# Kernel optimization log

Hardware: AMD Instinct MI355X
Metric: run time of the kernel (lower is better)

The kernel has to match this reference:

```python
import jax, jax.numpy as jnp
import numpy as np

N_GAUSS = 2048
FEAT_DIM = 3
IMG_H, IMG_W = 256, 256
EPS = 1e-4  # args.eps with tiled rasterizer path


def setup_inputs() -> dict:
    key = jax.random.key(0)
    k_xy, k_sc, k_rot, k_feat = jax.random.split(key, 4)
    xy = jax.random.uniform(k_xy, (N_GAUSS, 2), dtype=jnp.float32)  # normalized [0,1) coords
    # scale holds INVERSE std-devs (disable_inverse_scale=False path: scale = 1/init_scale);
    # values 10..50 give Gaussians spanning a few pixels at 256x256.
    scale = jax.random.uniform(k_sc, (N_GAUSS, 2), minval=10.0, maxval=50.0, dtype=jnp.float32)
    rot = jax.random.normal(k_rot, (N_GAUSS, 1), dtype=jnp.float32)
    feat = jax.random.uniform(k_feat, (N_GAUSS, FEAT_DIM), dtype=jnp.float32)
    return {"xy": xy, "scale": scale, "rot": rot, "feat": feat, "topk": 8}


def reference(xy, scale, rot, feat, topk):
    # Pixel centers in normalized coordinates, matching get_grid(h, w) -> (x, y)
    xs = (jnp.arange(IMG_W, dtype=jnp.float32) + 0.5) / IMG_W
    ys = (jnp.arange(IMG_H, dtype=jnp.float32) + 0.5) / IMG_H
    px, py = jnp.meshgrid(xs, ys, indexing="xy")  # each [H, W]
    px = px.reshape(-1)  # [P]
    py = py.reshape(-1)

    dx = px[:, None] - xy[None, :, 0]  # [P, N]
    dy = py[:, None] - xy[None, :, 1]  # [P, N]

    c = jnp.cos(rot[:, 0])  # [N]
    s = jnp.sin(rot[:, 0])
    # Rotate offset into the Gaussian's local frame
    lx = dx * c + dy * s   # [P, N]
    ly = -dx * s + dy * c  # [P, N]

    # Anisotropic Gaussian weight; scale is the inverse std-dev per axis
    w = jnp.exp(-0.5 * ((lx * scale[:, 0]) ** 2 + (ly * scale[:, 1]) ** 2))  # [P, N]

    # Keep top-k Gaussians per pixel, normalize their weights, accumulate features
    tw, ti = jax.lax.top_k(w, topk)        # [P, K]
    tf = feat[ti]                          # [P, K, C]
    alpha = tw / (jnp.sum(tw, axis=-1, keepdims=True) + EPS)  # [P, K]
    img = jnp.einsum("pk,pkc->pc", alpha, tf)                 # [P, C]
    return img.reshape(IMG_H, IMG_W, FEAT_DIM).transpose(2, 0, 1)  # [C, H, W]
```

## Files before the change

kernel.cpp:

```cpp
#include <hip/hip_runtime.h>
#include <math.h>

#define N_GAUSS 2048
#define IMG_H 256
#define IMG_W 256
#define NPIX (IMG_H * IMG_W)
#define EPS 1e-4f

#define TILE 8
#define TILES_X (IMG_W / TILE)
#define NTILES (TILES_X * (IMG_H / TILE))
#define SEG 512
#define D_HALF 0.019336f

#define LADDER(T, G)                                                     \
    if ((T) < v7) {                                                      \
        const bool c0 = (T) < v0, c1 = (T) < v1, c2 = (T) < v2;          \
        const bool c3 = (T) < v3, c4 = (T) < v4, c5 = (T) < v5;          \
        const bool c6 = (T) < v6;                                        \
        v7 = c6 ? v6 : (T);            i7 = c6 ? i6 : (G);               \
        v6 = c6 ? (c5 ? v5 : (T)) : v6; i6 = c6 ? (c5 ? i5 : (G)) : i6;  \
        v5 = c5 ? (c4 ? v4 : (T)) : v5; i5 = c5 ? (c4 ? i4 : (G)) : i5;  \
        v4 = c4 ? (c3 ? v3 : (T)) : v4; i4 = c4 ? (c3 ? i3 : (G)) : i4;  \
        v3 = c3 ? (c2 ? v2 : (T)) : v3; i3 = c3 ? (c2 ? i2 : (G)) : i3;  \
        v2 = c2 ? (c1 ? v1 : (T)) : v2; i2 = c2 ? (c1 ? i1 : (G)) : i2;  \
        v1 = c1 ? (c0 ? v0 : (T)) : v1; i1 = c1 ? (c0 ? i0 : (G)) : i1;  \
        v0 = c0 ? (T) : v0;            i0 = c0 ? (G) : i0;               \
    }

#define VLADDER(T)                                                       \
    if ((T) < v7) {                                                      \
        const bool c0 = (T) < v0, c1 = (T) < v1, c2 = (T) < v2;          \
        const bool c3 = (T) < v3, c4 = (T) < v4, c5 = (T) < v5;          \
        const bool c6 = (T) < v6;                                        \
        v7 = c6 ? v6 : (T);                                              \
        v6 = c6 ? (c5 ? v5 : (T)) : v6;                                  \
        v5 = c5 ? (c4 ? v4 : (T)) : v5;                                  \
        v4 = c4 ? (c3 ? v3 : (T)) : v4;                                  \
        v3 = c3 ? (c2 ? v2 : (T)) : v3;                                  \
        v2 = c2 ? (c1 ? v1 : (T)) : v2;                                  \
        v1 = c1 ? (c0 ? v0 : (T)) : v1;                                  \
        v0 = c0 ? (T) : v0;                                              \
    }

#define CE(a, i, j)                                   \
    { float lo_ = fminf(a[i], a[j]);                  \
      float hi_ = fmaxf(a[i], a[j]);                  \
      a[i] = lo_; a[j] = hi_; }

#define MERGE8(A, B)                                  \
    { float t_[8];                                    \
      t_[0] = fminf(A[0], B[7]); t_[1] = fminf(A[1], B[6]); \
      t_[2] = fminf(A[2], B[5]); t_[3] = fminf(A[3], B[4]); \
      t_[4] = fminf(A[4], B[3]); t_[5] = fminf(A[5], B[2]); \
      t_[6] = fminf(A[6], B[1]); t_[7] = fminf(A[7], B[0]); \
      CE(t_,0,4) CE(t_,1,5) CE(t_,2,6) CE(t_,3,7)     \
      CE(t_,0,2) CE(t_,1,3) CE(t_,4,6) CE(t_,5,7)     \
      CE(t_,0,1) CE(t_,2,3) CE(t_,4,5) CE(t_,6,7)     \
      A[0]=t_[0]; A[1]=t_[1]; A[2]=t_[2]; A[3]=t_[3]; \
      A[4]=t_[4]; A[5]=t_[5]; A[6]=t_[6]; A[7]=t_[7]; }

__launch_bounds__(256)
__global__ void fused_kernel(const float* __restrict__ xy,
                             const float* __restrict__ scale,
                             const float* __restrict__ rot,
                             const float* __restrict__ feat,
                             float* __restrict__ out) {
    __shared__ float rlo[N_GAUSS];
    __shared__ float wlist[4][8];
    __shared__ float s_cut;
    __shared__ unsigned short qidx[N_GAUSS];
    __shared__ int qcnt[4];
    __shared__ float          lt[4][8][64];
    __shared__ unsigned short li[4][8][64];

    const int tid  = threadIdx.x;
    const int lane = tid & 63;
    const int w    = tid >> 6;
    const int tile = blockIdx.x;

    const float cx = (float)((tile & (TILES_X - 1)) * TILE + 4) * (1.0f / IMG_W);
    const float cy = (float)((tile / TILES_X) * TILE + 4) * (1.0f / IMG_H);
    float cur[8];
    {
        float v0 = INFINITY, v1 = INFINITY, v2 = INFINITY, v3 = INFINITY;
        float v4 = INFINITY, v5 = INFINITY, v6 = INFINITY, v7 = INFINITY;
#pragma unroll
        for (int r = 0; r < N_GAUSS / 256; ++r) {
            int g = r * 256 + tid;
            float2 xyg = ((const float2*)xy)[g];
            float2 scg = ((const float2*)scale)[g];
            float  rg  = rot[g];
            float s, c;
            __sincosf(rg, &s, &c);
            float dx = cx - xyg.x;
            float dy = cy - xyg.y;
            float lx = dx * c + dy * s;
            float ly = dy * c - dx * s;
            float a  = lx * scg.x;
            float b  = ly * scg.y;
            float rr = sqrtf(a * a + b * b);
            float m  = fmaxf(scg.x, scg.y) * D_HALF;
            rlo[g]   = rr - m;
            float rp = rr + m;
            VLADDER(rp)
        }
        cur[0] = v0; cur[1] = v1; cur[2] = v2; cur[3] = v3;
        cur[4] = v4; cur[5] = v5; cur[6] = v6; cur[7] = v7;
    }

#pragma unroll
    for (int m = 1; m < 64; m <<= 1) {
        float oth[8];
#pragma unroll
        for (int k = 0; k < 8; ++k) oth[k] = __shfl_xor(cur[k], m, 64);
        float t_[8];
#pragma unroll
        for (int k = 0; k < 8; ++k) t_[k] = fminf(cur[k], oth[7 - k]);
        CE(t_,0,4) CE(t_,1,5) CE(t_,2,6) CE(t_,3,7)
        CE(t_,0,2) CE(t_,1,3) CE(t_,4,6) CE(t_,5,7)
        CE(t_,0,1) CE(t_,2,3) CE(t_,4,5) CE(t_,6,7)
#pragma unroll
        for (int k = 0; k < 8; ++k) cur[k] = t_[k];
    }
    if (lane == 0) {
#pragma unroll
        for (int k = 0; k < 8; ++k) wlist[w][k] = cur[k];
    }
    __syncthreads();

    if (tid == 0) {
        float A[8], B[8], C2[8], D2[8];
#pragma unroll
        for (int k = 0; k < 8; ++k) {
            A[k]  = wlist[0][k];
            B[k]  = wlist[1][k];
            C2[k] = wlist[2][k];
            D2[k] = wlist[3][k];
        }
        MERGE8(A, B)
        MERGE8(C2, D2)
        MERGE8(A, C2)
        float cut = A[7];
        s_cut = cut + 0.01f + 1e-4f * cut;
    }
    __syncthreads();
    const float cut = s_cut;

    {
        const int segbase = w * SEG;
        unsigned base = 0;
        for (int s2 = 0; s2 < SEG / 64; ++s2) {
            int g = segbase + s2 * 64 + lane;
            bool keep = rlo[g] <= cut;
            unsigned long long mask = __ballot(keep);
            unsigned pos = (unsigned)__popcll(mask & ((1ull << lane) - 1ull));
            if (keep) qidx[segbase + base + pos] = (unsigned short)g;
            base += (unsigned)__popcll(mask);
        }
        if (lane == 0) qcnt[w] = (int)base;
    }
    __syncthreads();

    const int pxi = (tile & (TILES_X - 1)) * TILE + (lane & 7);
    const int pyi = (tile / TILES_X) * TILE + (lane >> 3);
    const int p   = pyi * IMG_W + pxi;
    const float px = (pxi + 0.5f) * (1.0f / IMG_W);
    const float py = (pyi + 0.5f) * (1.0f / IMG_H);

    float v0 = INFINITY, v1 = INFINITY, v2 = INFINITY, v3 = INFINITY;
    float v4 = INFINITY, v5 = INFINITY, v6 = INFINITY, v7 = INFINITY;
    int   i0 = 0, i1 = 0, i2 = 0, i3 = 0, i4 = 0, i5 = 0, i6 = 0, i7 = 0;

    {
        const int segbase = w * SEG;
        const int cnt = qcnt[w];
        for (int b = 0; b < cnt; b += 64) {
            int t = b + lane;
            int gg = (t < cnt) ? (int)qidx[segbase + t] : 0;
            float2 xyg = ((const float2*)xy)[gg];
            float2 scg = ((const float2*)scale)[gg];
            double rg  = (double)rot[gg];
            float cc = (float)cos(rg);
            float ss = (float)sin(rg);
            int lim = cnt - b; if (lim > 64) lim = 64;
            for (int j = 0; j < lim; ++j) {
                float ax = __shfl(xyg.x, j, 64);
                float ay = __shfl(xyg.y, j, 64);
                float ac = __shfl(cc,    j, 64);
                float sn = __shfl(ss,    j, 64);
                float bx = __shfl(scg.x, j, 64);
                float by = __shfl(scg.y, j, 64);
                int   g  = __shfl(gg,    j, 64);
                float dx = __fsub_rn(px, ax);
                float dy = __fsub_rn(py, ay);
                float lx = __fadd_rn(__fmul_rn(dx, ac), __fmul_rn(dy, sn));
                float ly = __fadd_rn(__fmul_rn(-dx, sn), __fmul_rn(dy, ac));
                float aa = __fmul_rn(lx, bx);
                float bb = __fmul_rn(ly, by);
                float t2 = __fadd_rn(__fmul_rn(aa, aa), __fmul_rn(bb, bb));
                LADDER(t2, g)
            }
        }
    }

    lt[w][0][lane] = v0; li[w][0][lane] = (unsigned short)i0;
    lt[w][1][lane] = v1; li[w][1][lane] = (unsigned short)i1;
    lt[w][2][lane] = v2; li[w][2][lane] = (unsigned short)i2;
    lt[w][3][lane] = v3; li[w][3][lane] = (unsigned short)i3;
    lt[w][4][lane] = v4; li[w][4][lane] = (unsigned short)i4;
    lt[w][5][lane] = v5; li[w][5][lane] = (unsigned short)i5;
    lt[w][6][lane] = v6; li[w][6][lane] = (unsigned short)i6;
    lt[w][7][lane] = v7; li[w][7][lane] = (unsigned short)i7;
    __syncthreads();

    if (w == 0) {
        v0 = INFINITY; v1 = INFINITY; v2 = INFINITY; v3 = INFINITY;
        v4 = INFINITY; v5 = INFINITY; v6 = INFINITY; v7 = INFINITY;
        i0 = 0; i1 = 0; i2 = 0; i3 = 0; i4 = 0; i5 = 0; i6 = 0; i7 = 0;
        for (int c = 0; c < 4; ++c) {
#pragma unroll
            for (int k = 0; k < 8; ++k) {
                float t2 = lt[c][k][lane];
                int   g  = (int)li[c][k][lane];
                LADDER(t2, g)
            }
        }
        float w0 = expf(-0.5f * v0), w1 = expf(-0.5f * v1);
        float w2 = expf(-0.5f * v2), w3 = expf(-0.5f * v3);
        float w4 = expf(-0.5f * v4), w5 = expf(-0.5f * v5);
        float w6 = expf(-0.5f * v6), w7 = expf(-0.5f * v7);
        float sum = w0 + w1 + w2 + w3 + w4 + w5 + w6 + w7;
        float inv = 1.0f / (sum + EPS);

        float oc0 = 0.f, oc1 = 0.f, oc2 = 0.f;
#define ACC(K)                                                  \
        {                                                       \
            float al = w##K * inv;                              \
            const float* f = feat + 3 * i##K;                   \
            oc0 = fmaf(al, f[0], oc0);                          \
            oc1 = fmaf(al, f[1], oc1);                          \
            oc2 = fmaf(al, f[2], oc2);                          \
        }
        ACC(0) ACC(1) ACC(2) ACC(3) ACC(4) ACC(5) ACC(6) ACC(7)
#undef ACC

        out[p]            = oc0;
        out[p + NPIX]     = oc1;
        out[p + 2 * NPIX] = oc2;
    }
}

extern "C" void kernel_launch(void* const* d_in, const int* in_sizes, int n_in,
                              void* d_out, int out_size, void* d_ws, size_t ws_size,
                              hipStream_t stream) {
    const float* xy    = (const float*)d_in[0];
    const float* scale = (const float*)d_in[1];
    const float* rot   = (const float*)d_in[2];
    const float* feat  = (const float*)d_in[3];
    float* out = (float*)d_out;

    fused_kernel<<<NTILES, 256, 0, stream>>>(xy, scale, rot, feat, out);
}
```

Before: 24.74 us.

## Use 16x16 tiles with 1024-thread blocks and stage culled Gaussian params in LDS

```diff
diff --git a/kernel.cpp b/kernel.cpp
--- a/kernel.cpp
+++ b/kernel.cpp
@@ -7,11 +7,13 @@
 #define NPIX (IMG_H * IMG_W)
 #define EPS 1e-4f
 
-#define TILE 8
+#define TILE 16
 #define TILES_X (IMG_W / TILE)
 #define NTILES (TILES_X * (IMG_H / TILE))
-#define SEG 512
-#define D_HALF 0.019336f
+#define NTHREADS 1024
+#define NWAVES 16
+#define SEG (N_GAUSS / NWAVES)
+#define D_HALF 0.041436f
 
 #define LADDER(T, G)                                                     \
     if ((T) < v7) {                                                      \
@@ -48,46 +50,55 @@
       float hi_ = fmaxf(a[i], a[j]);                  \
       a[i] = lo_; a[j] = hi_; }
 
-#define MERGE8(A, B)                                  \
-    { float t_[8];                                    \
-      t_[0] = fminf(A[0], B[7]); t_[1] = fminf(A[1], B[6]); \
-      t_[2] = fminf(A[2], B[5]); t_[3] = fminf(A[3], B[4]); \
-      t_[4] = fminf(A[4], B[3]); t_[5] = fminf(A[5], B[2]); \
-      t_[6] = fminf(A[6], B[1]); t_[7] = fminf(A[7], B[0]); \
-      CE(t_,0,4) CE(t_,1,5) CE(t_,2,6) CE(t_,3,7)     \
-      CE(t_,0,2) CE(t_,1,3) CE(t_,4,6) CE(t_,5,7)     \
-      CE(t_,0,1) CE(t_,2,3) CE(t_,4,5) CE(t_,6,7)     \
-      A[0]=t_[0]; A[1]=t_[1]; A[2]=t_[2]; A[3]=t_[3]; \
-      A[4]=t_[4]; A[5]=t_[5]; A[6]=t_[6]; A[7]=t_[7]; }
-
-__launch_bounds__(256)
+__device__ __forceinline__ void top8_butterfly(float (&cur)[8]) {
+#pragma unroll
+    for (int m = 1; m < 64; m <<= 1) {
+        float oth[8];
+#pragma unroll
+        for (int k = 0; k < 8; ++k) oth[k] = __shfl_xor(cur[k], m, 64);
+        float t_[8];
+#pragma unroll
+        for (int k = 0; k < 8; ++k) t_[k] = fminf(cur[k], oth[7 - k]);
+        CE(t_,0,4) CE(t_,1,5) CE(t_,2,6) CE(t_,3,7)
+        CE(t_,0,2) CE(t_,1,3) CE(t_,4,6) CE(t_,5,7)
+        CE(t_,0,1) CE(t_,2,3) CE(t_,4,5) CE(t_,6,7)
+#pragma unroll
+        for (int k = 0; k < 8; ++k) cur[k] = t_[k];
+    }
+}
+
+__launch_bounds__(NTHREADS)
 __global__ void fused_kernel(const float* __restrict__ xy,
                              const float* __restrict__ scale,
                              const float* __restrict__ rot,
                              const float* __restrict__ feat,
                              float* __restrict__ out) {
     __shared__ float rlo[N_GAUSS];
-    __shared__ float wlist[4][8];
+    __shared__ float wlist[NWAVES][8];
     __shared__ float s_cut;
     __shared__ unsigned short qidx[N_GAUSS];
-    __shared__ int qcnt[4];
-    __shared__ float          lt[4][8][64];
-    __shared__ unsigned short li[4][8][64];
+    __shared__ int qcnt[NWAVES];
+    __shared__ float4 cps[N_GAUSS];
+    __shared__ float2 csc[N_GAUSS];
+    __shared__ float          lt[4][8][256];
+    __shared__ unsigned short li[4][8][256];
 
     const int tid  = threadIdx.x;
     const int lane = tid & 63;
     const int w    = tid >> 6;
     const int tile = blockIdx.x;
-
-    const float cx = (float)((tile & (TILES_X - 1)) * TILE + 4) * (1.0f / IMG_W);
-    const float cy = (float)((tile / TILES_X) * TILE + 4) * (1.0f / IMG_H);
+    const int tx   = tile & (TILES_X - 1);
+    const int ty   = tile >> 4;
+
+    const float cx = (float)(tx * TILE + 8) * (1.0f / IMG_W);
+    const float cy = (float)(ty * TILE + 8) * (1.0f / IMG_H);
     float cur[8];
     {
         float v0 = INFINITY, v1 = INFINITY, v2 = INFINITY, v3 = INFINITY;
         float v4 = INFINITY, v5 = INFINITY, v6 = INFINITY, v7 = INFINITY;
 #pragma unroll
-        for (int r = 0; r < N_GAUSS / 256; ++r) {
-            int g = r * 256 + tid;
+        for (int r = 0; r < N_GAUSS / NTHREADS; ++r) {
+            int g = r * NTHREADS + tid;
             float2 xyg = ((const float2*)xy)[g];
             float2 scg = ((const float2*)scale)[g];
             float  rg  = rot[g];
@@ -109,40 +120,23 @@
         cur[4] = v4; cur[5] = v5; cur[6] = v6; cur[7] = v7;
     }
 
-#pragma unroll
-    for (int m = 1; m < 64; m <<= 1) {
-        float oth[8];
-#pragma unroll
-        for (int k = 0; k < 8; ++k) oth[k] = __shfl_xor(cur[k], m, 64);
-        float t_[8];
-#pragma unroll
-        for (int k = 0; k < 8; ++k) t_[k] = fminf(cur[k], oth[7 - k]);
-        CE(t_,0,4) CE(t_,1,5) CE(t_,2,6) CE(t_,3,7)
-        CE(t_,0,2) CE(t_,1,3) CE(t_,4,6) CE(t_,5,7)
-        CE(t_,0,1) CE(t_,2,3) CE(t_,4,5) CE(t_,6,7)
-#pragma unroll
-        for (int k = 0; k < 8; ++k) cur[k] = t_[k];
-    }
+    top8_butterfly(cur);
     if (lane == 0) {
 #pragma unroll
         for (int k = 0; k < 8; ++k) wlist[w][k] = cur[k];
     }
     __syncthreads();
 
-    if (tid == 0) {
-        float A[8], B[8], C2[8], D2[8];
-#pragma unroll
-        for (int k = 0; k < 8; ++k) {
-            A[k]  = wlist[0][k];
-            B[k]  = wlist[1][k];
-            C2[k] = wlist[2][k];
-            D2[k] = wlist[3][k];
-        }
-        MERGE8(A, B)
-        MERGE8(C2, D2)
-        MERGE8(A, C2)
-        float cut = A[7];
-        s_cut = cut + 0.01f + 1e-4f * cut;
+    if (w == 0) {
+        float cur2[8];
+#pragma unroll
+        for (int k = 0; k < 8; ++k)
+            cur2[k] = (lane < NWAVES) ? wlist[lane][k] : INFINITY;
+        top8_butterfly(cur2);
+        if (lane == 0) {
+            float cut = cur2[7];
+            s_cut = cut + 0.01f + 1e-4f * cut;
+        }
     }
     __syncthreads();
     const float cut = s_cut;
@@ -154,16 +148,27 @@
             int g = segbase + s2 * 64 + lane;
             bool keep = rlo[g] <= cut;
             unsigned long long mask = __ballot(keep);
-            unsigned pos = (unsigned)__popcll(mask & ((1ull << lane) - 1ull));
-            if (keep) qidx[segbase + base + pos] = (unsigned short)g;
+            if (keep) {
+                unsigned pos = base + (unsigned)__popcll(mask & ((1ull << lane) - 1ull));
+                float2 xyg = ((const float2*)xy)[g];
+                float2 scg = ((const float2*)scale)[g];
+                double rg  = (double)rot[g];
+                float cc = (float)cos(rg);
+                float ss = (float)sin(rg);
+                qidx[segbase + pos] = (unsigned short)g;
+                cps[segbase + pos]  = make_float4(xyg.x, xyg.y, cc, ss);
+                csc[segbase + pos]  = make_float2(scg.x, scg.y);
+            }
             base += (unsigned)__popcll(mask);
         }
         if (lane == 0) qcnt[w] = (int)base;
     }
     __syncthreads();
 
-    const int pxi = (tile & (TILES_X - 1)) * TILE + (lane & 7);
-    const int pyi = (tile / TILES_X) * TILE + (lane >> 3);
+    const int st = w & 3;
+    const int q  = w >> 2;
+    const int pxi = tx * TILE + (st & 1) * 8 + (lane & 7);
+    const int pyi = ty * TILE + (st >> 1) * 8 + (lane >> 3);
     const int p   = pyi * IMG_W + pxi;
     const float px = (pxi + 0.5f) * (1.0f / IMG_W);
     const float py = (pyi + 0.5f) * (1.0f / IMG_H);
@@ -172,57 +177,47 @@
     float v4 = INFINITY, v5 = INFINITY, v6 = INFINITY, v7 = INFINITY;
     int   i0 = 0, i1 = 0, i2 = 0, i3 = 0, i4 = 0, i5 = 0, i6 = 0, i7 = 0;
 
+    for (int s = q * 4; s < q * 4 + 4; ++s) {
+        const int sb  = s * SEG;
+        const int cnt = qcnt[s];
+        for (int j = 0; j < cnt; ++j) {
+            float4 a4 = cps[sb + j];
+            float2 b2 = csc[sb + j];
+            int    g  = (int)qidx[sb + j];
+            float dx = __fsub_rn(px, a4.x);
+            float dy = __fsub_rn(py, a4.y);
+            float lx = __fadd_rn(__fmul_rn(dx, a4.z), __fmul_rn(dy, a4.w));
+            float ly = __fadd_rn(__fmul_rn(-dx, a4.w), __fmul_rn(dy, a4.z));
+            float aa = __fmul_rn(lx, b2.x);
+            float bb = __fmul_rn(ly, b2.y);
+            float t2 = __fadd_rn(__fmul_rn(aa, aa), __fmul_rn(bb, bb));
+            LADDER(t2, g)
+        }
+    }
+
     {
-        const int segbase = w * SEG;
-        const int cnt = qcnt[w];
-        for (int b = 0; b < cnt; b += 64) {
-            int t = b + lane;
-            int gg = (t < cnt) ? (int)qidx[segbase + t] : 0;
-            float2 xyg = ((const float2*)xy)[gg];
-            float2 scg = ((const float2*)scale)[gg];
-            double rg  = (double)rot[gg];
-            float cc = (float)cos(rg);
-            float ss = (float)sin(rg);
-            int lim = cnt - b; if (lim > 64) lim = 64;
-            for (int j = 0; j < lim; ++j) {
-                float ax = __shfl(xyg.x, j, 64);
-                float ay = __shfl(xyg.y, j, 64);
-                float ac = __shfl(cc,    j, 64);
-                float sn = __shfl(ss,    j, 64);
-                float bx = __shfl(scg.x, j, 64);
-                float by = __shfl(scg.y, j, 64);
-                int   g  = __shfl(gg,    j, 64);
-                float dx = __fsub_rn(px, ax);
-                float dy = __fsub_rn(py, ay);
-                float lx = __fadd_rn(__fmul_rn(dx, ac), __fmul_rn(dy, sn));
-                float ly = __fadd_rn(__fmul_rn(-dx, sn), __fmul_rn(dy, ac));
-                float aa = __fmul_rn(lx, bx);
-                float bb = __fmul_rn(ly, by);
-                float t2 = __fadd_rn(__fmul_rn(aa, aa), __fmul_rn(bb, bb));
-                LADDER(t2, g)
-            }
-        }
-    }
-
-    lt[w][0][lane] = v0; li[w][0][lane] = (unsigned short)i0;
-    lt[w][1][lane] = v1; li[w][1][lane] = (unsigned short)i1;
-    lt[w][2][lane] = v2; li[w][2][lane] = (unsigned short)i2;
-    lt[w][3][lane] = v3; li[w][3][lane] = (unsigned short)i3;
-    lt[w][4][lane] = v4; li[w][4][lane] = (unsigned short)i4;
-    lt[w][5][lane] = v5; li[w][5][lane] = (unsigned short)i5;
-    lt[w][6][lane] = v6; li[w][6][lane] = (unsigned short)i6;
-    lt[w][7][lane] = v7; li[w][7][lane] = (unsigned short)i7;
-    __syncthreads();
-
-    if (w == 0) {
+        const int pix = st * 64 + lane;
+        lt[q][0][pix] = v0; li[q][0][pix] = (unsigned short)i0;
+        lt[q][1][pix] = v1; li[q][1][pix] = (unsigned short)i1;
+        lt[q][2][pix] = v2; li[q][2][pix] = (unsigned short)i2;
+        lt[q][3][pix] = v3; li[q][3][pix] = (unsigned short)i3;
+        lt[q][4][pix] = v4; li[q][4][pix] = (unsigned short)i4;
+        lt[q][5][pix] = v5; li[q][5][pix] = (unsigned short)i5;
+        lt[q][6][pix] = v6; li[q][6][pix] = (unsigned short)i6;
+        lt[q][7][pix] = v7; li[q][7][pix] = (unsigned short)i7;
+    }
+    __syncthreads();
+
+    if (w < 4) {
         v0 = INFINITY; v1 = INFINITY; v2 = INFINITY; v3 = INFINITY;
         v4 = INFINITY; v5 = INFINITY; v6 = INFINITY; v7 = INFINITY;
         i0 = 0; i1 = 0; i2 = 0; i3 = 0; i4 = 0; i5 = 0; i6 = 0; i7 = 0;
+        const int pix = w * 64 + lane;
         for (int c = 0; c < 4; ++c) {
 #pragma unroll
             for (int k = 0; k < 8; ++k) {
-                float t2 = lt[c][k][lane];
-                int   g  = (int)li[c][k][lane];
+                float t2 = lt[c][k][pix];
+                int   g  = (int)li[c][k][pix];
                 LADDER(t2, g)
             }
         }
@@ -260,5 +255,5 @@
     const float* feat  = (const float*)d_in[3];
     float* out = (float*)d_out;
 
-    fused_kernel<<<NTILES, 256, 0, stream>>>(xy, scale, rot, feat, out);
+    fused_kernel<<<NTILES, NTHREADS, 0, stream>>>(xy, scale, rot, feat, out);
 }
```

Result: slower. 26.80 us (+8.3%).

## Precompute per-Gaussian params in prep kernel and stage candidates in LDS

Applied to the files above, without the earlier changes.

```diff
diff --git a/kernel.cpp b/kernel.cpp
--- a/kernel.cpp
+++ b/kernel.cpp
@@ -11,6 +11,7 @@
 #define TILES_X (IMG_W / TILE)
 #define NTILES (TILES_X * (IMG_H / TILE))
 #define SEG 512
+#define SEGCAP 128
 #define D_HALF 0.019336f
 
 #define LADDER(T, G)                                                     \
@@ -28,25 +29,18 @@
         v0 = c0 ? (T) : v0;            i0 = c0 ? (G) : i0;               \
     }
 
-#define VLADDER(T)                                                       \
-    if ((T) < v7) {                                                      \
-        const bool c0 = (T) < v0, c1 = (T) < v1, c2 = (T) < v2;          \
-        const bool c3 = (T) < v3, c4 = (T) < v4, c5 = (T) < v5;          \
-        const bool c6 = (T) < v6;                                        \
-        v7 = c6 ? v6 : (T);                                              \
-        v6 = c6 ? (c5 ? v5 : (T)) : v6;                                  \
-        v5 = c5 ? (c4 ? v4 : (T)) : v5;                                  \
-        v4 = c4 ? (c3 ? v3 : (T)) : v4;                                  \
-        v3 = c3 ? (c2 ? v2 : (T)) : v3;                                  \
-        v2 = c2 ? (c1 ? v1 : (T)) : v2;                                  \
-        v1 = c1 ? (c0 ? v0 : (T)) : v1;                                  \
-        v0 = c0 ? (T) : v0;                                              \
-    }
-
 #define CE(a, i, j)                                   \
     { float lo_ = fminf(a[i], a[j]);                  \
       float hi_ = fmaxf(a[i], a[j]);                  \
       a[i] = lo_; a[j] = hi_; }
+
+#define SORT8(a)                                      \
+    CE(a,0,1) CE(a,2,3) CE(a,4,5) CE(a,6,7)           \
+    CE(a,0,2) CE(a,1,3) CE(a,4,6) CE(a,5,7)           \
+    CE(a,1,2) CE(a,5,6)                               \
+    CE(a,0,4) CE(a,1,5) CE(a,2,6) CE(a,3,7)           \
+    CE(a,2,4) CE(a,3,5)                               \
+    CE(a,1,2) CE(a,3,4) CE(a,5,6)
 
 #define MERGE8(A, B)                                  \
     { float t_[8];                                    \
@@ -60,10 +54,48 @@
       A[0]=t_[0]; A[1]=t_[1]; A[2]=t_[2]; A[3]=t_[3]; \
       A[4]=t_[4]; A[5]=t_[5]; A[6]=t_[6]; A[7]=t_[7]; }
 
+__device__ __forceinline__ void top8_butterfly(float (&cur)[8]) {
+#pragma unroll
+    for (int m = 1; m < 64; m <<= 1) {
+        float oth[8];
+#pragma unroll
+        for (int k = 0; k < 8; ++k) oth[k] = __shfl_xor(cur[k], m, 64);
+        float t_[8];
+#pragma unroll
+        for (int k = 0; k < 8; ++k) t_[k] = fminf(cur[k], oth[7 - k]);
+        CE(t_,0,4) CE(t_,1,5) CE(t_,2,6) CE(t_,3,7)
+        CE(t_,0,2) CE(t_,1,3) CE(t_,4,6) CE(t_,5,7)
+        CE(t_,0,1) CE(t_,2,3) CE(t_,4,5) CE(t_,6,7)
+#pragma unroll
+        for (int k = 0; k < 8; ++k) cur[k] = t_[k];
+    }
+}
+
+__global__ void prep_kernel(const float* __restrict__ xy,
+                            const float* __restrict__ scale,
+                            const float* __restrict__ rot,
+                            float4* __restrict__ gA,
+                            float4* __restrict__ gB,
+                            float4* __restrict__ gC) {
+    int g = blockIdx.x * blockDim.x + threadIdx.x;
+    if (g >= N_GAUSS) return;
+    float x  = xy[2 * g + 0];
+    float y  = xy[2 * g + 1];
+    float sx = scale[2 * g + 0];
+    float sy = scale[2 * g + 1];
+    double r = (double)rot[g];
+    float c = (float)cos(r);
+    float s = (float)sin(r);
+    gA[g] = make_float4(x, y, c * sx, s * sx);
+    gB[g] = make_float4(-s * sy, c * sy, fmaxf(sx, sy) * D_HALF, 0.f);
+    gC[g] = make_float4(c, s, sx, sy);
+}
+
 __launch_bounds__(256)
 __global__ void fused_kernel(const float* __restrict__ xy,
-                             const float* __restrict__ scale,
-                             const float* __restrict__ rot,
+                             const float4* __restrict__ gA,
+                             const float4* __restrict__ gB,
+                             const float4* __restrict__ gC,
                              const float* __restrict__ feat,
                              float* __restrict__ out) {
     __shared__ float rlo[N_GAUSS];
@@ -71,6 +103,8 @@
     __shared__ float s_cut;
     __shared__ unsigned short qidx[N_GAUSS];
     __shared__ int qcnt[4];
+    __shared__ float4 cps[4 * SEGCAP];
+    __shared__ float2 csc[4 * SEGCAP];
     __shared__ float          lt[4][8][64];
     __shared__ unsigned short li[4][8][64];
 
@@ -82,47 +116,22 @@
     const float cx = (float)((tile & (TILES_X - 1)) * TILE + 4) * (1.0f / IMG_W);
     const float cy = (float)((tile / TILES_X) * TILE + 4) * (1.0f / IMG_H);
     float cur[8];
-    {
-        float v0 = INFINITY, v1 = INFINITY, v2 = INFINITY, v3 = INFINITY;
-        float v4 = INFINITY, v5 = INFINITY, v6 = INFINITY, v7 = INFINITY;
-#pragma unroll
-        for (int r = 0; r < N_GAUSS / 256; ++r) {
-            int g = r * 256 + tid;
-            float2 xyg = ((const float2*)xy)[g];
-            float2 scg = ((const float2*)scale)[g];
-            float  rg  = rot[g];
-            float s, c;
-            __sincosf(rg, &s, &c);
-            float dx = cx - xyg.x;
-            float dy = cy - xyg.y;
-            float lx = dx * c + dy * s;
-            float ly = dy * c - dx * s;
-            float a  = lx * scg.x;
-            float b  = ly * scg.y;
-            float rr = sqrtf(a * a + b * b);
-            float m  = fmaxf(scg.x, scg.y) * D_HALF;
-            rlo[g]   = rr - m;
-            float rp = rr + m;
-            VLADDER(rp)
-        }
-        cur[0] = v0; cur[1] = v1; cur[2] = v2; cur[3] = v3;
-        cur[4] = v4; cur[5] = v5; cur[6] = v6; cur[7] = v7;
-    }
-
-#pragma unroll
-    for (int m = 1; m < 64; m <<= 1) {
-        float oth[8];
-#pragma unroll
-        for (int k = 0; k < 8; ++k) oth[k] = __shfl_xor(cur[k], m, 64);
-        float t_[8];
-#pragma unroll
-        for (int k = 0; k < 8; ++k) t_[k] = fminf(cur[k], oth[7 - k]);
-        CE(t_,0,4) CE(t_,1,5) CE(t_,2,6) CE(t_,3,7)
-        CE(t_,0,2) CE(t_,1,3) CE(t_,4,6) CE(t_,5,7)
-        CE(t_,0,1) CE(t_,2,3) CE(t_,4,5) CE(t_,6,7)
-#pragma unroll
-        for (int k = 0; k < 8; ++k) cur[k] = t_[k];
-    }
+#pragma unroll
+    for (int r = 0; r < N_GAUSS / 256; ++r) {
+        int g = r * 256 + tid;
+        float4 a = gA[g];
+        float4 b = gB[g];
+        float dx = cx - a.x;
+        float dy = cy - a.y;
+        float lx = dx * a.z + dy * a.w;
+        float ly = dx * b.x + dy * b.y;
+        float rr = sqrtf(lx * lx + ly * ly);
+        rlo[g]  = rr - b.z;
+        cur[r]  = rr + b.z;
+    }
+    SORT8(cur)
+
+    top8_butterfly(cur);
     if (lane == 0) {
 #pragma unroll
         for (int k = 0; k < 8; ++k) wlist[w][k] = cur[k];
@@ -154,8 +163,16 @@
             int g = segbase + s2 * 64 + lane;
             bool keep = rlo[g] <= cut;
             unsigned long long mask = __ballot(keep);
-            unsigned pos = (unsigned)__popcll(mask & ((1ull << lane) - 1ull));
-            if (keep) qidx[segbase + base + pos] = (unsigned short)g;
+            if (keep) {
+                unsigned pos = base + (unsigned)__popcll(mask & ((1ull << lane) - 1ull));
+                qidx[segbase + pos] = (unsigned short)g;
+                if (pos < SEGCAP) {
+                    float4 a = gA[g];
+                    float4 e = gC[g];
+                    cps[w * SEGCAP + pos] = make_float4(a.x, a.y, e.x, e.y);
+                    csc[w * SEGCAP + pos] = make_float2(e.z, e.w);
+                }
+            }
             base += (unsigned)__popcll(mask);
         }
         if (lane == 0) qcnt[w] = (int)base;
@@ -172,37 +189,36 @@
     float v4 = INFINITY, v5 = INFINITY, v6 = INFINITY, v7 = INFINITY;
     int   i0 = 0, i1 = 0, i2 = 0, i3 = 0, i4 = 0, i5 = 0, i6 = 0, i7 = 0;
 
+#define PROC_EXACT(AX, AY, AC, AS, BX, BY, G)                            \
+    {                                                                    \
+        float dx = __fsub_rn(px, (AX));                                  \
+        float dy = __fsub_rn(py, (AY));                                  \
+        float lx = __fadd_rn(__fmul_rn(dx, (AC)), __fmul_rn(dy, (AS)));  \
+        float ly = __fadd_rn(__fmul_rn(-dx, (AS)), __fmul_rn(dy, (AC))); \
+        float aa = __fmul_rn(lx, (BX));                                  \
+        float bb = __fmul_rn(ly, (BY));                                  \
+        float t2 = __fadd_rn(__fmul_rn(aa, aa), __fmul_rn(bb, bb));      \
+        LADDER(t2, (G))                                                  \
+    }
+
     {
         const int segbase = w * SEG;
-        const int cnt = qcnt[w];
-        for (int b = 0; b < cnt; b += 64) {
-            int t = b + lane;
-            int gg = (t < cnt) ? (int)qidx[segbase + t] : 0;
-            float2 xyg = ((const float2*)xy)[gg];
-            float2 scg = ((const float2*)scale)[gg];
-            double rg  = (double)rot[gg];
-            float cc = (float)cos(rg);
-            float ss = (float)sin(rg);
-            int lim = cnt - b; if (lim > 64) lim = 64;
-            for (int j = 0; j < lim; ++j) {
-                float ax = __shfl(xyg.x, j, 64);
-                float ay = __shfl(xyg.y, j, 64);
-                float ac = __shfl(cc,    j, 64);
-                float sn = __shfl(ss,    j, 64);
-                float bx = __shfl(scg.x, j, 64);
-                float by = __shfl(scg.y, j, 64);
-                int   g  = __shfl(gg,    j, 64);
-                float dx = __fsub_rn(px, ax);
-                float dy = __fsub_rn(py, ay);
-                float lx = __fadd_rn(__fmul_rn(dx, ac), __fmul_rn(dy, sn));
-                float ly = __fadd_rn(__fmul_rn(-dx, sn), __fmul_rn(dy, ac));
-                float aa = __fmul_rn(lx, bx);
-                float bb = __fmul_rn(ly, by);
-                float t2 = __fadd_rn(__fmul_rn(aa, aa), __fmul_rn(bb, bb));
-                LADDER(t2, g)
-            }
-        }
-    }
+        const int cnt  = qcnt[w];
+        const int jcap = cnt < SEGCAP ? cnt : SEGCAP;
+        for (int j = 0; j < jcap; ++j) {
+            float4 a4 = cps[w * SEGCAP + j];
+            float2 b2 = csc[w * SEGCAP + j];
+            int    g  = (int)qidx[segbase + j];
+            PROC_EXACT(a4.x, a4.y, a4.z, a4.w, b2.x, b2.y, g)
+        }
+        for (int j = SEGCAP; j < cnt; ++j) {
+            int    g  = (int)qidx[segbase + j];
+            float4 a  = gA[g];
+            float4 e  = gC[g];
+            PROC_EXACT(a.x, a.y, e.x, e.y, e.z, e.w, g)
+        }
+    }
+#undef PROC_EXACT
 
     lt[w][0][lane] = v0; li[w][0][lane] = (unsigned short)i0;
     lt[w][1][lane] = v1; li[w][1][lane] = (unsigned short)i1;
@@ -260,5 +276,10 @@
     const float* feat  = (const float*)d_in[3];
     float* out = (float*)d_out;
 
-    fused_kernel<<<NTILES, 256, 0, stream>>>(xy, scale, rot, feat, out);
-}
+    float4* gA = (float4*)d_ws;
+    float4* gB = gA + N_GAUSS;
+    float4* gC = gB + N_GAUSS;
+
+    prep_kernel<<<N_GAUSS / 256, 256, 0, stream>>>(xy, scale, rot, gA, gB, gC);
+    fused_kernel<<<NTILES, 256, 0, stream>>>(xy, gA, gB, gC, feat, out);
+}
```

Measured after the change: 27.45 us. +10.9%, slower.
